# Optimization experiments

Measured on AMD Instinct MI355X. Metric: run time of the kernel, lower is better.

The kernel has to match this reference:

```python
import math
import jax, jax.numpy as jnp
import numpy as np

SCALE = 64.0
MARGIN = 0.5
T = 0.2
COS_M = math.cos(MARGIN)
SIN_M = math.sin(MARGIN)
TH = math.cos(math.pi - MARGIN)
MM = math.sin(math.pi - MARGIN) * MARGIN
EPS = 1e-07

B, D, C = 512, 512, 100000


def setup_inputs() -> dict:
    key = jax.random.key(0)
    k1, k2, k3 = jax.random.split(key, 3)
    embedding = jax.random.normal(k1, (B, D), dtype=jnp.float32)
    # xavier_uniform for (num_classes, embed_size)
    limit = math.sqrt(6.0 / (C + D))
    weight = jax.random.uniform(k2, (C, D), dtype=jnp.float32, minval=-limit, maxval=limit)
    ground_truth = jax.random.randint(k3, (B,), 0, C, dtype=jnp.int64)
    return {"embedding": embedding, "weight": weight, "ground_truth": ground_truth}


def reference(embedding, weight, ground_truth):
    gt = ground_truth.astype(jnp.int32)
    e = embedding / jnp.linalg.norm(embedding, axis=1, keepdims=True)
    w = weight / jnp.linalg.norm(weight, axis=1, keepdims=True)
    # (B, C) cosine similarities
    cos_theta = jnp.clip(jnp.einsum('bd,cd->bc', e, w), -1.0 + EPS, 1.0 - EPS)
    pos = jnp.take_along_axis(cos_theta, gt[:, None], axis=1)  # (B, 1)
    sin_theta = jnp.sqrt(jnp.clip(1.0 - pos * pos, EPS, 1.0 - EPS))
    phi = pos * COS_M - sin_theta * SIN_M
    phi = jnp.where(pos > TH, phi, pos - MM)  # easy_margin=False branch
    # hard-example reweighting: fixed=False -> (t+1)*cos + t where cos > phi
    mask = cos_theta > phi  # phi broadcasts (B,1) -> (B,C)
    cos_theta = jnp.where(mask, (T + 1.0) * cos_theta + T, cos_theta)
    # scatter phi into the ground-truth column
    output = cos_theta.at[jnp.arange(B), gt].set(phi[:, 0])
    output = output * SCALE
    # mean cross-entropy
    logp = jax.nn.log_softmax(output, axis=1)
    loss = -jnp.mean(jnp.take_along_axis(logp, gt[:, None], axis=1))
    return loss
```

## Files before the change

kernel.cpp:

```cpp
#include <hip/hip_runtime.h>
#include <hip/hip_bf16.h>
#include <stdint.h>

typedef unsigned short u16;
typedef __attribute__((ext_vector_type(8))) short short8;
typedef __attribute__((ext_vector_type(4))) float floatx4;

#define B_   512
#define D_   512
#define C_   100000

#define SCALE_  64.0f
#define COSM_   0.8775825618903728f
#define SINM_   0.479425538604203f
#define TH_     (-0.8775825618903728f)
#define MM_     0.2397127693021015f
#define EPS_    1e-7f
#define SHIFT_  89.6f

#define BM 256
#define BN 64
#define BK 32

__device__ inline float wave_reduce_sum(float v) {
    v += __shfl_xor(v, 1);
    v += __shfl_xor(v, 2);
    v += __shfl_xor(v, 4);
    v += __shfl_xor(v, 8);
    v += __shfl_xor(v, 16);
    v += __shfl_xor(v, 32);
    return v;
}

__device__ inline u16 f2bf(float x) {
    union { float f; uint32_t u; } v; v.f = x;
    uint32_t r = v.u + 0x7fffu + ((v.u >> 16) & 1u);
    return (u16)(r >> 16);
}

__global__ __launch_bounds__(256) void norm_e_phi_kernel(
    const float* __restrict__ emb, const float* __restrict__ w_raw,
    const int* __restrict__ gt, u16* __restrict__ e_bf16,
    float* __restrict__ phi, float* __restrict__ rowsum) {
    if (threadIdx.x < 4) rowsum[blockIdx.x * 4 + threadIdx.x] = 0.0f;
    int wv = threadIdx.x >> 6;
    int lane = threadIdx.x & 63;
    int b = blockIdx.x * 4 + wv;
    const float4* rp = (const float4*)(emb + (long)b * D_);
    float4 f0 = rp[lane], f1 = rp[lane + 64];
    float sq = f0.x*f0.x + f0.y*f0.y + f0.z*f0.z + f0.w*f0.w
             + f1.x*f1.x + f1.y*f1.y + f1.z*f1.z + f1.w*f1.w;
    sq = wave_reduce_sum(sq);
    float rn = 1.0f / sqrtf(sq);
    f0.x *= rn; f0.y *= rn; f0.z *= rn; f0.w *= rn;
    f1.x *= rn; f1.y *= rn; f1.z *= rn; f1.w *= rn;
    uint2 p0, p1;
    p0.x = (uint32_t)f2bf(f0.x) | ((uint32_t)f2bf(f0.y) << 16);
    p0.y = (uint32_t)f2bf(f0.z) | ((uint32_t)f2bf(f0.w) << 16);
    p1.x = (uint32_t)f2bf(f1.x) | ((uint32_t)f2bf(f1.y) << 16);
    p1.y = (uint32_t)f2bf(f1.z) | ((uint32_t)f2bf(f1.w) << 16);
    uint2* ob = (uint2*)(e_bf16 + (long)b * D_);
    ob[lane] = p0;
    ob[lane + 64] = p1;

    int g = gt[b];
    const float4* wp = (const float4*)(w_raw + (long)g * D_);
    float4 w0 = wp[lane], w1 = wp[lane + 64];
    float dt = f0.x*w0.x + f0.y*w0.y + f0.z*w0.z + f0.w*w0.w
             + f1.x*w1.x + f1.y*w1.y + f1.z*w1.z + f1.w*w1.w;
    float wsq = w0.x*w0.x + w0.y*w0.y + w0.z*w0.z + w0.w*w0.w
              + w1.x*w1.x + w1.y*w1.y + w1.z*w1.z + w1.w*w1.w;
    dt = wave_reduce_sum(dt);
    wsq = wave_reduce_sum(wsq);
    if (lane == 0) {
        float pos = dt / sqrtf(wsq);
        pos = fminf(fmaxf(pos, -1.0f + EPS_), 1.0f - EPS_);
        float s2 = 1.0f - pos * pos;
        s2 = fminf(fmaxf(s2, EPS_), 1.0f - EPS_);
        float sin_t = sqrtf(s2);
        float ph = pos * COSM_ - sin_t * SINM_;
        ph = (pos > TH_) ? ph : (pos - MM_);
        phi[b] = ph;
    }
}

__device__ inline void cvt_store(const float4& v0, const float4& v1,
                                 u16* dst, float& sq) {
    union { u16 h[8]; uint4 q; } u;
    u.h[0] = f2bf(v0.x); u.h[1] = f2bf(v0.y);
    u.h[2] = f2bf(v0.z); u.h[3] = f2bf(v0.w);
    u.h[4] = f2bf(v1.x); u.h[5] = f2bf(v1.y);
    u.h[6] = f2bf(v1.z); u.h[7] = f2bf(v1.w);
    *(uint4*)dst = u.q;
    sq += v0.x*v0.x + v0.y*v0.y + v0.z*v0.z + v0.w*v0.w
        + v1.x*v1.x + v1.y*v1.y + v1.z*v1.z + v1.w*v1.w;
}

__global__ __launch_bounds__(256, 3) void gemm_arcface_fused(
    const u16* __restrict__ a_g,
    const float* __restrict__ w_g,
    const float* __restrict__ phi, const int* __restrict__ gt,
    float* __restrict__ rowsum) {
    __shared__ __align__(16) u16 b_tile[2][BN * BK];
    __shared__ float phi_s[BM];
    __shared__ int gt_s[BM];
    __shared__ float rnorm_s[BN];

    int tid = threadIdx.x;
    int c0 = (blockIdx.x >> 1) * BN;
    int m0 = (blockIdx.x & 1) * BM;

    phi_s[tid] = phi[m0 + tid];
    gt_s[tid] = gt[m0 + tid];

    int rb = tid >> 2;
    int bslot = tid & 3;
    int bkq = bslot ^ ((rb >> 1) & 3);
    long brow_g = min(c0 + rb, C_ - 1);
    const float4* b_src = (const float4*)(w_g + brow_g * (long)D_ + bkq * 8);
    u16* b_dst0 = &b_tile[0][rb * BK + bslot * 8];
    u16* b_dst1 = &b_tile[1][rb * BK + bslot * 8];

    int wv = tid >> 6, lane = tid & 63;
    int low4 = lane & 15, quad = lane >> 4;
    int lslot = quad ^ ((low4 >> 1) & 3);
    const u16* a_base = a_g + (long)(m0 + wv * 64 + low4) * D_ + quad * 8;
    int bf_off = low4 * BK + lslot * 8;

    floatx4 acc[4][4] = {};
    float sq = 0.0f;
    float4 bv[4][2];
    short8 afc[4];

#pragma unroll
    for (int j = 0; j < 4; j++) {
        bv[j][0] = b_src[j * 8];
        bv[j][1] = b_src[j * 8 + 1];
    }
    cvt_store(bv[0][0], bv[0][1], b_dst0, sq);
    asm volatile("s_waitcnt lgkmcnt(0)" ::: "memory");
    __builtin_amdgcn_s_barrier();

#pragma unroll
    for (int kt = 0; kt < 16; kt++) {
        int p = kt & 1;
        if (kt < 12) {
            bv[kt & 3][0] = b_src[(kt + 4) * 8];
            bv[kt & 3][1] = b_src[(kt + 4) * 8 + 1];
        }
#pragma unroll
        for (int mi = 0; mi < 4; mi++)
            afc[mi] = *(const short8*)(a_base + (long)mi * 16 * D_ + kt * BK);
        short8 bf[4];
#pragma unroll
        for (int ni = 0; ni < 4; ni++)
            bf[ni] = *(const short8*)(&b_tile[p][ni * 16 * BK + bf_off]);
#pragma unroll
        for (int mi = 0; mi < 4; mi++)
#pragma unroll
            for (int ni = 0; ni < 4; ni++)
                acc[mi][ni] = __builtin_amdgcn_mfma_f32_16x16x32_bf16(
                    afc[mi], bf[ni], acc[mi][ni], 0, 0, 0);
        if (kt < 15)
            cvt_store(bv[(kt + 1) & 3][0], bv[(kt + 1) & 3][1],
                      p ? b_dst0 : b_dst1, sq);
        asm volatile("s_waitcnt lgkmcnt(0)" ::: "memory");
        __builtin_amdgcn_s_barrier();
    }

    sq += __shfl_xor(sq, 1);
    sq += __shfl_xor(sq, 2);
    if ((tid & 3) == 0) rnorm_s[rb] = 1.0f / sqrtf(sq);
    __syncthreads();

#pragma unroll
    for (int mi = 0; mi < 4; mi++) {
#pragma unroll
        for (int r = 0; r < 4; r++) {
            int rl = wv * 64 + mi * 16 + quad * 4 + r;
            float ph = phi_s[rl];
            int g = gt_s[rl];
            float s = 0.0f;
#pragma unroll
            for (int ni = 0; ni < 4; ni++) {
                int cl = ni * 16 + low4;
                int c = c0 + cl;
                float v = acc[mi][ni][r] * rnorm_s[cl];
                v = fminf(fmaxf(v, -1.0f + EPS_), 1.0f - EPS_);
                float logit = (v > ph) ? (1.2f * v + 0.2f) : v;
                logit *= SCALE_;
                if (c == g) logit = SCALE_ * ph;
                s += (c < C_) ? __expf(logit - SHIFT_) : 0.0f;
            }
            s += __shfl_xor(s, 1);
            s += __shfl_xor(s, 2);
            s += __shfl_xor(s, 4);
            s += __shfl_xor(s, 8);
            if (low4 == 0) atomicAdd(&rowsum[m0 + rl], s);
        }
    }
}

__global__ __launch_bounds__(256) void loss_kernel(
    const float* __restrict__ rowsum, const float* __restrict__ phi,
    float* __restrict__ out) {
    __shared__ float red[4];
    int tid = threadIdx.x;
    float s = 0.0f;
    for (int b = tid; b < B_; b += 256)
        s += logf(rowsum[b]) + SHIFT_ - SCALE_ * phi[b];
    s = wave_reduce_sum(s);
    int wv = tid >> 6, lane = tid & 63;
    if (lane == 0) red[wv] = s;
    __syncthreads();
    if (tid == 0) out[0] = (red[0] + red[1] + red[2] + red[3]) * (1.0f / B_);
}

extern "C" void kernel_launch(void* const* d_in, const int* in_sizes, int n_in,
                              void* d_out, int out_size, void* d_ws, size_t ws_size,
                              hipStream_t stream) {
    const float* emb = (const float*)d_in[0];
    const float* wgt = (const float*)d_in[1];
    const int* gt = (const int*)d_in[2];
    float* out = (float*)d_out;

    char* ws = (char*)d_ws;
    u16* e_bf16 = (u16*)(ws);
    float* phi = (float*)(ws + 524288);
    float* rowsum = (float*)(ws + 526336);

    norm_e_phi_kernel<<<B_ / 4, 256, 0, stream>>>(emb, wgt, gt, e_bf16, phi, rowsum);
    int nc = (C_ + BN - 1) / BN;
    gemm_arcface_fused<<<nc * 2, 256, 0, stream>>>(e_bf16, wgt, phi, gt, rowsum);
    loss_kernel<<<1, 256, 0, stream>>>(rowsum, phi, out);
}
```

Measured before the change: 444.9 us.

## Pre-tile bf16 embedding into MFMA fragment layout and coalesce weight loads

The normalize kernel now writes the bf16 embedding in a fragment-ordered layout, so each wave's A-operand load in the GEMM is one contiguous 1KB read per MFMA tile instead of strided row reads. Weight tile loading is reorganized so eight consecutive lanes read one contiguous 128-byte row segment, each thread covering two rows. The per-row norm reduction now spans eight lanes. Conversion uses the packed bf16x2 round-to-nearest intrinsic instead of manual bit rounding. The main cost targeted is uncoalesced global loads of the fp32 weight stream and the A fragments, at the price of more complex swizzle index math.

```diff
diff --git a/kernel.cpp b/kernel.cpp
--- a/kernel.cpp
+++ b/kernel.cpp
@@ -36,6 +36,12 @@
     union { float f; uint32_t u; } v; v.f = x;
     uint32_t r = v.u + 0x7fffu + ((v.u >> 16) & 1u);
     return (u16)(r >> 16);
+}
+
+__device__ inline uint32_t cvt2_rn(float a, float b) {
+    union { __hip_bfloat162 h; uint32_t u; } v;
+    v.h = __float22bfloat162_rn(make_float2(a, b));
+    return v.u;
 }
 
 __global__ __launch_bounds__(256) void norm_e_phi_kernel(
@@ -59,9 +65,10 @@
     p0.y = (uint32_t)f2bf(f0.z) | ((uint32_t)f2bf(f0.w) << 16);
     p1.x = (uint32_t)f2bf(f1.x) | ((uint32_t)f2bf(f1.y) << 16);
     p1.y = (uint32_t)f2bf(f1.z) | ((uint32_t)f2bf(f1.w) << 16);
-    uint2* ob = (uint2*)(e_bf16 + (long)b * D_);
-    ob[lane] = p0;
-    ob[lane + 64] = p1;
+    size_t d0 = (size_t)((((b >> 6) * 16 + (lane >> 3)) * 4 + ((b >> 4) & 3))) * 512
+              + (size_t)((((lane >> 1) & 3) * 16 + (b & 15)) * 8) + (lane & 1) * 4;
+    *(uint2*)(e_bf16 + d0) = p0;
+    *(uint2*)(e_bf16 + d0 + 16384) = p1;
 
     int g = gt[b];
     const float4* wp = (const float4*)(w_raw + (long)g * D_);
@@ -84,16 +91,14 @@
     }
 }
 
-__device__ inline void cvt_store(const float4& v0, const float4& v1,
-                                 u16* dst, float& sq) {
-    union { u16 h[8]; uint4 q; } u;
-    u.h[0] = f2bf(v0.x); u.h[1] = f2bf(v0.y);
-    u.h[2] = f2bf(v0.z); u.h[3] = f2bf(v0.w);
-    u.h[4] = f2bf(v1.x); u.h[5] = f2bf(v1.y);
-    u.h[6] = f2bf(v1.z); u.h[7] = f2bf(v1.w);
-    *(uint4*)dst = u.q;
-    sq += v0.x*v0.x + v0.y*v0.y + v0.z*v0.z + v0.w*v0.w
-        + v1.x*v1.x + v1.y*v1.y + v1.z*v1.z + v1.w*v1.w;
+__device__ inline void cvt_store2(const float4& a, const float4& b,
+                                  u16* dA, u16* dB, float& sqa, float& sqb) {
+    uint2 ua; ua.x = cvt2_rn(a.x, a.y); ua.y = cvt2_rn(a.z, a.w);
+    uint2 ub; ub.x = cvt2_rn(b.x, b.y); ub.y = cvt2_rn(b.z, b.w);
+    *(uint2*)dA = ua;
+    *(uint2*)dB = ub;
+    sqa += a.x*a.x + a.y*a.y + a.z*a.z + a.w*a.w;
+    sqb += b.x*b.x + b.y*b.y + b.z*b.z + b.w*b.w;
 }
 
 __global__ __launch_bounds__(256, 3) void gemm_arcface_fused(
@@ -113,31 +118,34 @@
     phi_s[tid] = phi[m0 + tid];
     gt_s[tid] = gt[m0 + tid];
 
-    int rb = tid >> 2;
-    int bslot = tid & 3;
-    int bkq = bslot ^ ((rb >> 1) & 3);
-    long brow_g = min(c0 + rb, C_ - 1);
-    const float4* b_src = (const float4*)(w_g + brow_g * (long)D_ + bkq * 8);
-    u16* b_dst0 = &b_tile[0][rb * BK + bslot * 8];
-    u16* b_dst1 = &b_tile[1][rb * BK + bslot * 8];
-
     int wv = tid >> 6, lane = tid & 63;
     int low4 = lane & 15, quad = lane >> 4;
+
+    int rA = wv * 16 + (lane >> 3);
+    long growA = min(c0 + rA, C_ - 1);
+    long growB = min(c0 + rA + 8, C_ - 1);
+    const float4* srcA = (const float4*)(w_g + growA * (long)D_) + (lane & 7);
+    const float4* srcB = (const float4*)(w_g + growB * (long)D_) + (lane & 7);
+    int physU = ((lane & 7) >> 1) ^ ((lane >> 4) & 3);
+    int stoff = physU * 8 + (lane & 1) * 4;
+    u16* dA[2] = { &b_tile[0][rA * 32 + stoff], &b_tile[1][rA * 32 + stoff] };
+    u16* dB[2] = { &b_tile[0][(rA + 8) * 32 + stoff], &b_tile[1][(rA + 8) * 32 + stoff] };
+
+    const u16* a2w = a_g + (size_t)((m0 >> 6) + wv) * 32768;
+
     int lslot = quad ^ ((low4 >> 1) & 3);
-    const u16* a_base = a_g + (long)(m0 + wv * 64 + low4) * D_ + quad * 8;
     int bf_off = low4 * BK + lslot * 8;
 
     floatx4 acc[4][4] = {};
-    float sq = 0.0f;
+    float sqA = 0.0f, sqB = 0.0f;
     float4 bv[4][2];
-    short8 afc[4];
 
 #pragma unroll
     for (int j = 0; j < 4; j++) {
-        bv[j][0] = b_src[j * 8];
-        bv[j][1] = b_src[j * 8 + 1];
-    }
-    cvt_store(bv[0][0], bv[0][1], b_dst0, sq);
+        bv[j][0] = srcA[j * 8];
+        bv[j][1] = srcB[j * 8];
+    }
+    cvt_store2(bv[0][0], bv[0][1], dA[0], dB[0], sqA, sqB);
     asm volatile("s_waitcnt lgkmcnt(0)" ::: "memory");
     __builtin_amdgcn_s_barrier();
 
@@ -145,12 +153,13 @@
     for (int kt = 0; kt < 16; kt++) {
         int p = kt & 1;
         if (kt < 12) {
-            bv[kt & 3][0] = b_src[(kt + 4) * 8];
-            bv[kt & 3][1] = b_src[(kt + 4) * 8 + 1];
+            bv[kt & 3][0] = srcA[(kt + 4) * 8];
+            bv[kt & 3][1] = srcB[(kt + 4) * 8];
         }
+        short8 af[4];
 #pragma unroll
         for (int mi = 0; mi < 4; mi++)
-            afc[mi] = *(const short8*)(a_base + (long)mi * 16 * D_ + kt * BK);
+            af[mi] = *(const short8*)(a2w + ((kt * 4 + mi) << 9) + (lane << 3));
         short8 bf[4];
 #pragma unroll
         for (int ni = 0; ni < 4; ni++)
@@ -160,17 +169,20 @@
 #pragma unroll
             for (int ni = 0; ni < 4; ni++)
                 acc[mi][ni] = __builtin_amdgcn_mfma_f32_16x16x32_bf16(
-                    afc[mi], bf[ni], acc[mi][ni], 0, 0, 0);
+                    af[mi], bf[ni], acc[mi][ni], 0, 0, 0);
         if (kt < 15)
-            cvt_store(bv[(kt + 1) & 3][0], bv[(kt + 1) & 3][1],
-                      p ? b_dst0 : b_dst1, sq);
+            cvt_store2(bv[(kt + 1) & 3][0], bv[(kt + 1) & 3][1],
+                       dA[1 - p], dB[1 - p], sqA, sqB);
         asm volatile("s_waitcnt lgkmcnt(0)" ::: "memory");
         __builtin_amdgcn_s_barrier();
     }
 
-    sq += __shfl_xor(sq, 1);
-    sq += __shfl_xor(sq, 2);
-    if ((tid & 3) == 0) rnorm_s[rb] = 1.0f / sqrtf(sq);
+    sqA += __shfl_xor(sqA, 1); sqA += __shfl_xor(sqA, 2); sqA += __shfl_xor(sqA, 4);
+    sqB += __shfl_xor(sqB, 1); sqB += __shfl_xor(sqB, 2); sqB += __shfl_xor(sqB, 4);
+    if ((lane & 7) == 0) {
+        rnorm_s[rA] = 1.0f / sqrtf(sqA);
+        rnorm_s[rA + 8] = 1.0f / sqrtf(sqB);
+    }
     __syncthreads();
 
 #pragma unroll
```

New measurement: 515.7 us. +15.9%, slower.

## Make GEMM blocks loop over class-tile chunks and reduce rowsums via partial buffer

Applied to the files above, without the earlier changes.

Each GEMM block now walks four consecutive 64-class tiles and keeps its per-row exp sums in registers, instead of handling one tile and issuing atomics for every tile. The grid shrinks from about 3126 to 782 blocks. When the workspace is large enough, per-chunk partial sums go to a padded buffer and a new reduce kernel sums them, which replaces the per-tile atomicAdd contention. The bf16 conversion also switches to the packed __float22bfloat162_rn intrinsic. The trade-off is fewer blocks in flight to cover the tail, plus one extra kernel launch.

```diff
diff --git a/kernel.cpp b/kernel.cpp
--- a/kernel.cpp
+++ b/kernel.cpp
@@ -21,6 +21,10 @@
 #define BM 256
 #define BN 64
 #define BK 32
+#define NTILES 1563
+#define CHUNK  4
+#define NCH    391
+#define PADP   392
 
 __device__ inline float wave_reduce_sum(float v) {
     v += __shfl_xor(v, 1);
@@ -36,6 +40,12 @@
     union { float f; uint32_t u; } v; v.f = x;
     uint32_t r = v.u + 0x7fffu + ((v.u >> 16) & 1u);
     return (u16)(r >> 16);
+}
+
+__device__ inline uint32_t cvt2_rn(float a, float b) {
+    union { __hip_bfloat162 h; uint32_t u; } v;
+    v.h = __float22bfloat162_rn(make_float2(a, b));
+    return v.u;
 }
 
 __global__ __launch_bounds__(256) void norm_e_phi_kernel(
@@ -86,12 +96,12 @@
 
 __device__ inline void cvt_store(const float4& v0, const float4& v1,
                                  u16* dst, float& sq) {
-    union { u16 h[8]; uint4 q; } u;
-    u.h[0] = f2bf(v0.x); u.h[1] = f2bf(v0.y);
-    u.h[2] = f2bf(v0.z); u.h[3] = f2bf(v0.w);
-    u.h[4] = f2bf(v1.x); u.h[5] = f2bf(v1.y);
-    u.h[6] = f2bf(v1.z); u.h[7] = f2bf(v1.w);
-    *(uint4*)dst = u.q;
+    uint4 q;
+    q.x = cvt2_rn(v0.x, v0.y);
+    q.y = cvt2_rn(v0.z, v0.w);
+    q.z = cvt2_rn(v1.x, v1.y);
+    q.w = cvt2_rn(v1.z, v1.w);
+    *(uint4*)dst = q;
     sq += v0.x*v0.x + v0.y*v0.y + v0.z*v0.z + v0.w*v0.w
         + v1.x*v1.x + v1.y*v1.y + v1.z*v1.z + v1.w*v1.w;
 }
@@ -100,15 +110,16 @@
     const u16* __restrict__ a_g,
     const float* __restrict__ w_g,
     const float* __restrict__ phi, const int* __restrict__ gt,
-    float* __restrict__ rowsum) {
+    float* __restrict__ rowsum, float* __restrict__ partial) {
     __shared__ __align__(16) u16 b_tile[2][BN * BK];
     __shared__ float phi_s[BM];
     __shared__ int gt_s[BM];
     __shared__ float rnorm_s[BN];
 
     int tid = threadIdx.x;
-    int c0 = (blockIdx.x >> 1) * BN;
+    int chunk = blockIdx.x >> 1;
     int m0 = (blockIdx.x & 1) * BM;
+    int nt = min(CHUNK, NTILES - chunk * CHUNK);
 
     phi_s[tid] = phi[m0 + tid];
     gt_s[tid] = gt[m0 + tid];
@@ -116,8 +127,6 @@
     int rb = tid >> 2;
     int bslot = tid & 3;
     int bkq = bslot ^ ((rb >> 1) & 3);
-    long brow_g = min(c0 + rb, C_ - 1);
-    const float4* b_src = (const float4*)(w_g + brow_g * (long)D_ + bkq * 8);
     u16* b_dst0 = &b_tile[0][rb * BK + bslot * 8];
     u16* b_dst1 = &b_tile[1][rb * BK + bslot * 8];
 
@@ -127,78 +136,120 @@
     const u16* a_base = a_g + (long)(m0 + wv * 64 + low4) * D_ + quad * 8;
     int bf_off = low4 * BK + lslot * 8;
 
-    floatx4 acc[4][4] = {};
-    float sq = 0.0f;
-    float4 bv[4][2];
-    short8 afc[4];
-
-#pragma unroll
-    for (int j = 0; j < 4; j++) {
-        bv[j][0] = b_src[j * 8];
-        bv[j][1] = b_src[j * 8 + 1];
-    }
-    cvt_store(bv[0][0], bv[0][1], b_dst0, sq);
-    asm volatile("s_waitcnt lgkmcnt(0)" ::: "memory");
-    __builtin_amdgcn_s_barrier();
-
-#pragma unroll
-    for (int kt = 0; kt < 16; kt++) {
-        int p = kt & 1;
-        if (kt < 12) {
-            bv[kt & 3][0] = b_src[(kt + 4) * 8];
-            bv[kt & 3][1] = b_src[(kt + 4) * 8 + 1];
-        }
-#pragma unroll
-        for (int mi = 0; mi < 4; mi++)
-            afc[mi] = *(const short8*)(a_base + (long)mi * 16 * D_ + kt * BK);
-        short8 bf[4];
-#pragma unroll
-        for (int ni = 0; ni < 4; ni++)
-            bf[ni] = *(const short8*)(&b_tile[p][ni * 16 * BK + bf_off]);
-#pragma unroll
-        for (int mi = 0; mi < 4; mi++)
-#pragma unroll
-            for (int ni = 0; ni < 4; ni++)
-                acc[mi][ni] = __builtin_amdgcn_mfma_f32_16x16x32_bf16(
-                    afc[mi], bf[ni], acc[mi][ni], 0, 0, 0);
-        if (kt < 15)
-            cvt_store(bv[(kt + 1) & 3][0], bv[(kt + 1) & 3][1],
-                      p ? b_dst0 : b_dst1, sq);
+    float rs[4][4] = {{0.0f}};
+
+#pragma unroll 1
+    for (int ct = 0; ct < nt; ct++) {
+        int c0 = (chunk * CHUNK + ct) * BN;
+        long brow_g = min(c0 + rb, C_ - 1);
+        const float4* b_src = (const float4*)(w_g + brow_g * (long)D_ + bkq * 8);
+
+        floatx4 acc[4][4] = {};
+        float sq = 0.0f;
+        float4 bv[4][2];
+        short8 afc[4];
+
+#pragma unroll
+        for (int j = 0; j < 4; j++) {
+            bv[j][0] = b_src[j * 8];
+            bv[j][1] = b_src[j * 8 + 1];
+        }
+        cvt_store(bv[0][0], bv[0][1], b_dst0, sq);
         asm volatile("s_waitcnt lgkmcnt(0)" ::: "memory");
         __builtin_amdgcn_s_barrier();
+
+#pragma unroll
+        for (int kt = 0; kt < 16; kt++) {
+            int p = kt & 1;
+            if (kt < 12) {
+                bv[kt & 3][0] = b_src[(kt + 4) * 8];
+                bv[kt & 3][1] = b_src[(kt + 4) * 8 + 1];
+            }
+#pragma unroll
+            for (int mi = 0; mi < 4; mi++)
+                afc[mi] = *(const short8*)(a_base + (long)mi * 16 * D_ + kt * BK);
+            short8 bf[4];
+#pragma unroll
+            for (int ni = 0; ni < 4; ni++)
+                bf[ni] = *(const short8*)(&b_tile[p][ni * 16 * BK + bf_off]);
+#pragma unroll
+            for (int mi = 0; mi < 4; mi++)
+#pragma unroll
+                for (int ni = 0; ni < 4; ni++)
+                    acc[mi][ni] = __builtin_amdgcn_mfma_f32_16x16x32_bf16(
+                        afc[mi], bf[ni], acc[mi][ni], 0, 0, 0);
+            if (kt < 15)
+                cvt_store(bv[(kt + 1) & 3][0], bv[(kt + 1) & 3][1],
+                          p ? b_dst0 : b_dst1, sq);
+            asm volatile("s_waitcnt lgkmcnt(0)" ::: "memory");
+            __builtin_amdgcn_s_barrier();
+        }
+
+        sq += __shfl_xor(sq, 1);
+        sq += __shfl_xor(sq, 2);
+        if ((tid & 3) == 0) rnorm_s[rb] = 1.0f / sqrtf(sq);
+        __syncthreads();
+
+#pragma unroll
+        for (int mi = 0; mi < 4; mi++) {
+#pragma unroll
+            for (int r = 0; r < 4; r++) {
+                int rl = wv * 64 + mi * 16 + quad * 4 + r;
+                float ph = phi_s[rl];
+                int g = gt_s[rl];
+                float s = 0.0f;
+#pragma unroll
+                for (int ni = 0; ni < 4; ni++) {
+                    int cl = ni * 16 + low4;
+                    int c = c0 + cl;
+                    float v = acc[mi][ni][r] * rnorm_s[cl];
+                    v = fminf(fmaxf(v, -1.0f + EPS_), 1.0f - EPS_);
+                    float logit = (v > ph) ? (1.2f * v + 0.2f) : v;
+                    logit *= SCALE_;
+                    if (c == g) logit = SCALE_ * ph;
+                    s += (c < C_) ? __expf(logit - SHIFT_) : 0.0f;
+                }
+                s += __shfl_xor(s, 1);
+                s += __shfl_xor(s, 2);
+                s += __shfl_xor(s, 4);
+                s += __shfl_xor(s, 8);
+                rs[mi][r] += s;
+            }
+        }
     }
 
-    sq += __shfl_xor(sq, 1);
-    sq += __shfl_xor(sq, 2);
-    if ((tid & 3) == 0) rnorm_s[rb] = 1.0f / sqrtf(sq);
-    __syncthreads();
-
-#pragma unroll
-    for (int mi = 0; mi < 4; mi++) {
-#pragma unroll
-        for (int r = 0; r < 4; r++) {
-            int rl = wv * 64 + mi * 16 + quad * 4 + r;
-            float ph = phi_s[rl];
-            int g = gt_s[rl];
-            float s = 0.0f;
-#pragma unroll
-            for (int ni = 0; ni < 4; ni++) {
-                int cl = ni * 16 + low4;
-                int c = c0 + cl;
-                float v = acc[mi][ni][r] * rnorm_s[cl];
-                v = fminf(fmaxf(v, -1.0f + EPS_), 1.0f - EPS_);
-                float logit = (v > ph) ? (1.2f * v + 0.2f) : v;
-                logit *= SCALE_;
-                if (c == g) logit = SCALE_ * ph;
-                s += (c < C_) ? __expf(logit - SHIFT_) : 0.0f;
-            }
-            s += __shfl_xor(s, 1);
-            s += __shfl_xor(s, 2);
-            s += __shfl_xor(s, 4);
-            s += __shfl_xor(s, 8);
-            if (low4 == 0) atomicAdd(&rowsum[m0 + rl], s);
+    if (partial) {
+        if (low4 == 0) {
+#pragma unroll
+            for (int mi = 0; mi < 4; mi++)
+#pragma unroll
+                for (int r = 0; r < 4; r++) {
+                    int rl = wv * 64 + mi * 16 + quad * 4 + r;
+                    partial[(long)(m0 + rl) * PADP + chunk] = rs[mi][r];
+                }
+        }
+    } else {
+        if (low4 == 0) {
+#pragma unroll
+            for (int mi = 0; mi < 4; mi++)
+#pragma unroll
+                for (int r = 0; r < 4; r++) {
+                    int rl = wv * 64 + mi * 16 + quad * 4 + r;
+                    atomicAdd(&rowsum[m0 + rl], rs[mi][r]);
+                }
         }
     }
+}
+
+__global__ __launch_bounds__(256) void reduce_rowsum_kernel(
+    const float* __restrict__ partial, float* __restrict__ rowsum) {
+    int wv = threadIdx.x >> 6, lane = threadIdx.x & 63;
+    int b = blockIdx.x * 4 + wv;
+    const float* p = partial + (long)b * PADP;
+    float s = 0.0f;
+    for (int i = lane; i < NCH; i += 64) s += p[i];
+    s = wave_reduce_sum(s);
+    if (lane == 0) rowsum[b] = s;
 }
 
 __global__ __launch_bounds__(256) void loss_kernel(
@@ -228,9 +279,12 @@
     u16* e_bf16 = (u16*)(ws);
     float* phi = (float*)(ws + 524288);
     float* rowsum = (float*)(ws + 526336);
+    size_t need = 528384 + (size_t)B_ * PADP * 4;
+    float* partial = (ws_size >= need) ? (float*)(ws + 528384) : nullptr;
 
     norm_e_phi_kernel<<<B_ / 4, 256, 0, stream>>>(emb, wgt, gt, e_bf16, phi, rowsum);
-    int nc = (C_ + BN - 1) / BN;
-    gemm_arcface_fused<<<nc * 2, 256, 0, stream>>>(e_bf16, wgt, phi, gt, rowsum);
+    gemm_arcface_fused<<<NCH * 2, 256, 0, stream>>>(e_bf16, wgt, phi, gt, rowsum, partial);
+    if (partial)
+        reduce_rowsum_kernel<<<B_ / 4, 256, 0, stream>>>(partial, rowsum);
     loss_kernel<<<1, 256, 0, stream>>>(rowsum, phi, out);
 }
```

Result: slower. 712.5 us (+60.1%).
